# Kernel optimization log

Measured on AMD Instinct MI355X. Metric: run time of the kernel, lower is better.

The kernel has to match this reference:

```python
import jax, jax.numpy as jnp
import numpy as np

B, R, CIN, J, O, ITERS = 512, 1152, 8, 10, 16, 3  # batch, routes, in_ch, capsules, out_ch, routing iters


def squash(s, axis):
    # v = (||s||^2 / (1 + ||s||^2)) * s / ||s||  (standard CapsNet squash)
    sq = jnp.sum(s * s, axis=axis, keepdims=True)
    return (sq / (1.0 + sq)) * s * jax.lax.rsqrt(sq + 1e-8)


def setup_inputs() -> dict:
    key = jax.random.key(0)
    k1, k2 = jax.random.split(key)
    x = jax.random.normal(k1, (B, R, CIN), dtype=jnp.float32)
    W = jax.random.normal(k2, (R, J, O, CIN), dtype=jnp.float32)  # param, batch-broadcast
    return {"x": x, "W": W}


def reference(x, W):
    # u_hat[b,r,j,:] = W[r,j] @ x[b,r]   (replaces torch stack/cat broadcasting)
    u_hat = jnp.einsum('rjoc,brc->brjo', W, x)  # [B,R,J,O]
    b_ij = jnp.zeros((x.shape[0], R, J), dtype=x.dtype)
    v = None
    for it in range(ITERS):
        c_ij = jax.nn.softmax(b_ij, axis=2)                 # softmax over capsules j
        s_j = jnp.einsum('brj,brjo->bjo', c_ij, u_hat)      # weighted sum over routes
        v = squash(s_j, axis=-1)                            # [B,J,O]
        if it < ITERS - 1:
            b_ij = b_ij + jnp.einsum('brjo,bjo->brj', u_hat, v)  # agreement
    # torch returns v_j.squeeze(1) with shape [B, J, O, 1]
    return v[..., None]
```

## Files before the change

kernel.cpp:

```cpp
#include <hip/hip_runtime.h>
#include <cstdint>
#include <cstddef>

#define NB 512
#define NR 1152
#define NC 8
#define NJ 10
#define NO 16
#define NJO 160

typedef unsigned int uint32;

__device__ __forceinline__ uint32 f2bf(float f) {
    uint32 x = __float_as_uint(f);
    return (x + 0x7fffu + ((x >> 16) & 1u)) >> 16;
}
__device__ __forceinline__ float bflo(uint32 w) { return __uint_as_float(w << 16); }
__device__ __forceinline__ float bfhi(uint32 w) { return __uint_as_float(w & 0xffff0000u); }

__global__ __launch_bounds__(256) void xpose_kernel(const float* __restrict__ x,
                                                    float* __restrict__ xT) {
    const int r0 = blockIdx.x * 16;
    const int b0 = blockIdx.y * 64;
    const int t  = threadIdx.x;
    __shared__ float tile[16][65][8];

    for (int i = t; i < 2048; i += 256) {
        int b = i >> 5, r = (i >> 1) & 15, h = i & 1;
        float4 v = *(const float4*)&x[(size_t)(b0 + b) * (NR * NC) + (size_t)(r0 + r) * NC + h * 4];
        *(float4*)&tile[r][b][h * 4] = v;
    }
    __syncthreads();
    for (int i = t; i < 2048; i += 256) {
        int r = i >> 7, b = (i >> 1) & 63, h = i & 1;
        float4 v = *(const float4*)&tile[r][b][h * 4];
        *(float4*)&xT[(size_t)(r0 + r) * (NB * NC) + (size_t)(b0 + b) * NC + h * 4] = v;
    }
}

__global__ __launch_bounds__(320) void uhat_kernel(const float* __restrict__ xT,
                                                   const float* __restrict__ W,
                                                   uint32* __restrict__ u) {
    const int r = blockIdx.x;
    const int t = threadIdx.x;

    __shared__ float Ws[NC][NJO];
    __shared__ float xs[NB][NC];

    for (int i = t; i < NJO * NC; i += 320) {
        Ws[i & 7][i >> 3] = W[(size_t)r * (NJO * NC) + i];
    }
    {
        const float4* xsrc = (const float4*)(xT + (size_t)r * (NB * NC));
        float4* xdst = (float4*)&xs[0][0];
        for (int i = t; i < (NB * NC) / 4; i += 320) xdst[i] = xsrc[i];
    }
    __syncthreads();

    const int jo2  = t % 80;
    const int half = t / 80;

    float w0[8], w1[8];
#pragma unroll
    for (int c = 0; c < 8; ++c) {
        w0[c] = Ws[c][2 * jo2];
        w1[c] = Ws[c][2 * jo2 + 1];
    }

    for (int b = half; b < NB; b += 4) {
        const float4* xp = (const float4*)xs[b];
        float4 xa = xp[0], xb = xp[1];
        float a0 = w0[0] * xa.x + w0[1] * xa.y + w0[2] * xa.z + w0[3] * xa.w
                 + w0[4] * xb.x + w0[5] * xb.y + w0[6] * xb.z + w0[7] * xb.w;
        float a1 = w1[0] * xa.x + w1[1] * xa.y + w1[2] * xa.z + w1[3] * xa.w
                 + w1[4] * xb.x + w1[5] * xb.y + w1[6] * xb.z + w1[7] * xb.w;
        uint32 p = f2bf(a0) | (f2bf(a1) << 16);
        u[(size_t)(b * NR + r) * 80 + jo2] = p;
    }
}

template <int MODE>
__global__ __launch_bounds__(576, 2) void pass_kernel(const uint32* __restrict__ u,
                                                      float* __restrict__ vacc,
                                                      float* __restrict__ outp) {
    const int b  = blockIdx.x;
    const int t  = threadIdx.x;
    const int w  = t >> 6;
    const int l  = t & 63;
    const int m  = (l >> 2) & 15;
    const int qt = l & 3;

    __shared__ float vls[NJO];
    __shared__ float sl[NJO];
    for (int i = t; i < NJO; i += 576) {
        sl[i] = 0.0f;
        if (MODE != 0) vls[i] = vacc[b * NJO + i];
    }
    __syncthreads();

    float acc[40];
#pragma unroll
    for (int i = 0; i < 40; ++i) acc[i] = 0.0f;

    const uint32* ubase = u + (size_t)b * (NR * 80);

#pragma unroll 1
    for (int c8 = 0; c8 < 8; ++c8) {
        const int r = (w * 8 + c8) * 16 + m;
        const uint32* up = ubase + r * 80 + 2 * qt;

        uint32 ur[20];
#pragma unroll
        for (int j = 0; j < NJ; ++j) {
            uint2 q = *(const uint2*)(up + 8 * j);
            ur[2 * j]     = q.x;
            ur[2 * j + 1] = q.y;
        }

        float cj[NJ];
        if (MODE == 0) {
#pragma unroll
            for (int j = 0; j < NJ; ++j) cj[j] = 0.1f;
        } else {
            float sum = 0.0f;
#pragma unroll
            for (int j = 0; j < NJ; ++j) {
                float4 vv = *(const float4*)&vls[16 * j + 4 * qt];
                float pj = bflo(ur[2 * j]) * vv.x + bfhi(ur[2 * j]) * vv.y
                         + bflo(ur[2 * j + 1]) * vv.z + bfhi(ur[2 * j + 1]) * vv.w;
                pj += __shfl_xor(pj, 1);
                pj += __shfl_xor(pj, 2);
                float e = __expf(pj);
                cj[j] = e;
                sum += e;
            }
            float inv = 1.0f / sum;
#pragma unroll
            for (int j = 0; j < NJ; ++j) cj[j] *= inv;
        }

#pragma unroll
        for (int j = 0; j < NJ; ++j) {
            acc[4 * j + 0] += cj[j] * bflo(ur[2 * j]);
            acc[4 * j + 1] += cj[j] * bfhi(ur[2 * j]);
            acc[4 * j + 2] += cj[j] * bflo(ur[2 * j + 1]);
            acc[4 * j + 3] += cj[j] * bfhi(ur[2 * j + 1]);
        }
    }

    float a[24];
    {
        const int bit = (l >> 2) & 1;
#pragma unroll
        for (int i = 0; i < 24; ++i) {
            float lo = acc[i];
            float hi = (i + 24 < 40) ? acc[i + 24] : 0.0f;
            float send = bit ? lo : hi;
            float recv = __shfl_xor(send, 4);
            a[i] = (bit ? hi : lo) + recv;
        }
    }
#pragma unroll
    for (int st = 1; st < 4; ++st) {
        const int h = 24 >> st;
        const int bit = (l >> (2 + st)) & 1;
#pragma unroll
        for (int i = 0; i < 12; ++i) {
            if (i < h) {
                float send = bit ? a[i] : a[i + h];
                float recv = __shfl_xor(send, 4 << st);
                a[i] = (bit ? a[i + h] : a[i]) + recv;
            }
        }
    }
    const int base = 3 * (__brev((uint32)m) >> 28);
#pragma unroll
    for (int i = 0; i < 3; ++i) {
        int aidx = base + i;
        if (aidx < 40) {
            int j = aidx >> 2, e = aidx & 3;
            atomicAdd(&sl[16 * j + 4 * qt + e], a[i]);
        }
    }
    __syncthreads();

    if (t < 80) {
        float2 sv = *(const float2*)&sl[2 * t];
        float sq = sv.x * sv.x + sv.y * sv.y;
#pragma unroll
        for (int off = 1; off < 8; off <<= 1) sq += __shfl_xor(sq, off, 8);
        float scale = (sq / (1.0f + sq)) * rsqrtf(sq + 1e-8f);
        float vx = sv.x * scale, vy = sv.y * scale;
        if (MODE == 2) {
            *(float2*)&outp[b * NJO + 2 * t] = make_float2(vx, vy);
        } else if (MODE == 1) {
            float2 va = *(const float2*)&vacc[b * NJO + 2 * t];
            *(float2*)&vacc[b * NJO + 2 * t] = make_float2(va.x + vx, va.y + vy);
        } else {
            *(float2*)&vacc[b * NJO + 2 * t] = make_float2(vx, vy);
        }
    }
}

extern "C" void kernel_launch(void* const* d_in, const int* in_sizes, int n_in,
                              void* d_out, int out_size, void* d_ws, size_t ws_size,
                              hipStream_t stream) {
    (void)in_sizes; (void)n_in; (void)out_size; (void)ws_size;

    const float* x = (const float*)d_in[0];
    const float* W = (const float*)d_in[1];
    float* out = (float*)d_out;

    char* ws = (char*)d_ws;
    const size_t XBYTES = (size_t)NR * NB * NC * 4;
    const size_t UBYTES = (size_t)NB * NR * NJO * 2;
    float*  xT   = (float*)ws;
    uint32* u    = (uint32*)(ws + XBYTES);
    float*  vacc = (float*)(ws + XBYTES + UBYTES);

    xpose_kernel<<<dim3(NR / 16, NB / 64), 256, 0, stream>>>(x, xT);
    uhat_kernel<<<NR, 320, 0, stream>>>(xT, W, u);

    pass_kernel<0><<<NB, 576, 0, stream>>>(u, vacc, nullptr);
    pass_kernel<1><<<NB, 576, 0, stream>>>(u, vacc, nullptr);
    pass_kernel<2><<<NB, 576, 0, stream>>>(u, vacc, out);
}
```

Baseline: 231.0 us.

## Fuse three routing passes into one kernel with fp16 u_hat and vectorized loads

Merges the three per-iteration pass kernels into a single routing kernel that loops over iterations, keeping the accumulated v in shared memory instead of a global vacc buffer. u_hat is stored as fp16 instead of bf16, with the element order permuted so each thread's 20 words are contiguous and can be read with five 16-byte loads. The u_hat array is still re-read from global memory or L2 on every iteration. The aim is to remove two kernel launches and the global vacc round trips and to widen the loads. fp16 has a narrower range than bf16, which could overflow for large u_hat values.

```diff
diff --git a/kernel.cpp b/kernel.cpp
--- a/kernel.cpp
+++ b/kernel.cpp
@@ -1,4 +1,5 @@
 #include <hip/hip_runtime.h>
+#include <hip/hip_fp16.h>
 #include <cstdint>
 #include <cstddef>
 
@@ -11,12 +12,17 @@
 
 typedef unsigned int uint32;
 
-__device__ __forceinline__ uint32 f2bf(float f) {
-    uint32 x = __float_as_uint(f);
-    return (x + 0x7fffu + ((x >> 16) & 1u)) >> 16;
-}
-__device__ __forceinline__ float bflo(uint32 w) { return __uint_as_float(w << 16); }
-__device__ __forceinline__ float bfhi(uint32 w) { return __uint_as_float(w & 0xffff0000u); }
+union H2U { __half2 h; uint32 u; };
+
+__device__ __forceinline__ uint32 packf16(float a0, float a1) {
+    H2U p;
+    p.h = __halves2half2(__float2half_rn(a0), __float2half_rn(a1));
+    return p.u;
+}
+__device__ __forceinline__ float2 unpackf16(uint32 w) {
+    H2U p; p.u = w;
+    return __half22float2(p.h);
+}
 
 __global__ __launch_bounds__(256) void xpose_kernel(const float* __restrict__ x,
                                                     float* __restrict__ xT) {
@@ -44,7 +50,7 @@
     const int r = blockIdx.x;
     const int t = threadIdx.x;
 
-    __shared__ float Ws[NC][NJO];
+    __shared__ float Ws[NC][NJO + 4];
     __shared__ float xs[NB][NC];
 
     for (int i = t; i < NJO * NC; i += 320) {
@@ -57,14 +63,19 @@
     }
     __syncthreads();
 
-    const int jo2  = t % 80;
+    const int ni   = t % 80;
     const int half = t / 80;
+    const int qt  = ni / 20;
+    const int rem = ni % 20;
+    const int j   = rem >> 1;
+    const int d   = rem & 1;
+    const int jo0 = 16 * j + 4 * qt + 2 * d;
 
     float w0[8], w1[8];
 #pragma unroll
     for (int c = 0; c < 8; ++c) {
-        w0[c] = Ws[c][2 * jo2];
-        w1[c] = Ws[c][2 * jo2 + 1];
+        w0[c] = Ws[c][jo0];
+        w1[c] = Ws[c][jo0 + 1];
     }
 
     for (int b = half; b < NB; b += 4) {
@@ -74,15 +85,12 @@
                  + w0[4] * xb.x + w0[5] * xb.y + w0[6] * xb.z + w0[7] * xb.w;
         float a1 = w1[0] * xa.x + w1[1] * xa.y + w1[2] * xa.z + w1[3] * xa.w
                  + w1[4] * xb.x + w1[5] * xb.y + w1[6] * xb.z + w1[7] * xb.w;
-        uint32 p = f2bf(a0) | (f2bf(a1) << 16);
-        u[(size_t)(b * NR + r) * 80 + jo2] = p;
-    }
-}
-
-template <int MODE>
-__global__ __launch_bounds__(576, 2) void pass_kernel(const uint32* __restrict__ u,
-                                                      float* __restrict__ vacc,
-                                                      float* __restrict__ outp) {
+        u[(size_t)(b * NR + r) * 80 + ni] = packf16(a0, a1);
+    }
+}
+
+__global__ __launch_bounds__(576, 2) void routing_kernel(const uint32* __restrict__ u,
+                                                         float* __restrict__ outp) {
     const int b  = blockIdx.x;
     const int t  = threadIdx.x;
     const int w  = t >> 6;
@@ -90,114 +98,127 @@
     const int m  = (l >> 2) & 15;
     const int qt = l & 3;
 
+    __shared__ float sl[NJO];
     __shared__ float vls[NJO];
-    __shared__ float sl[NJO];
-    for (int i = t; i < NJO; i += 576) {
-        sl[i] = 0.0f;
-        if (MODE != 0) vls[i] = vacc[b * NJO + i];
-    }
+    __shared__ float vaccl[NJO];
+
+    for (int i = t; i < NJO; i += 576) sl[i] = 0.0f;
     __syncthreads();
 
-    float acc[40];
-#pragma unroll
-    for (int i = 0; i < 40; ++i) acc[i] = 0.0f;
-
-    const uint32* ubase = u + (size_t)b * (NR * 80);
+    const uint32* ubase = u + (size_t)b * (NR * 80) + qt * 20;
 
 #pragma unroll 1
-    for (int c8 = 0; c8 < 8; ++c8) {
-        const int r = (w * 8 + c8) * 16 + m;
-        const uint32* up = ubase + r * 80 + 2 * qt;
-
-        uint32 ur[20];
-#pragma unroll
-        for (int j = 0; j < NJ; ++j) {
-            uint2 q = *(const uint2*)(up + 8 * j);
-            ur[2 * j]     = q.x;
-            ur[2 * j + 1] = q.y;
-        }
-
-        float cj[NJ];
-        if (MODE == 0) {
-#pragma unroll
-            for (int j = 0; j < NJ; ++j) cj[j] = 0.1f;
-        } else {
-            float sum = 0.0f;
+    for (int it = 0; it < 3; ++it) {
+        float acc[40];
+#pragma unroll
+        for (int i = 0; i < 40; ++i) acc[i] = 0.0f;
+
+#pragma unroll 1
+        for (int c8 = 0; c8 < 8; ++c8) {
+            const int r = (w * 8 + c8) * 16 + m;
+            const uint4* up = (const uint4*)(ubase + (size_t)r * 80);
+            uint32 ur[20];
+#pragma unroll
+            for (int i = 0; i < 5; ++i) {
+                uint4 q = up[i];
+                ur[4 * i + 0] = q.x; ur[4 * i + 1] = q.y;
+                ur[4 * i + 2] = q.z; ur[4 * i + 3] = q.w;
+            }
+
+            float cj[NJ];
+            if (it == 0) {
+#pragma unroll
+                for (int j = 0; j < NJ; ++j) cj[j] = 0.1f;
+            } else {
+                float sum = 0.0f;
+#pragma unroll
+                for (int j = 0; j < NJ; ++j) {
+                    float2 ua = unpackf16(ur[2 * j]);
+                    float2 ub = unpackf16(ur[2 * j + 1]);
+                    float4 vv = *(const float4*)&vls[16 * j + 4 * qt];
+                    float pj = ua.x * vv.x + ua.y * vv.y + ub.x * vv.z + ub.y * vv.w;
+                    pj += __shfl_xor(pj, 1);
+                    pj += __shfl_xor(pj, 2);
+                    float e = __expf(pj);
+                    cj[j] = e;
+                    sum += e;
+                }
+                float inv = 1.0f / sum;
+#pragma unroll
+                for (int j = 0; j < NJ; ++j) cj[j] *= inv;
+            }
+
 #pragma unroll
             for (int j = 0; j < NJ; ++j) {
-                float4 vv = *(const float4*)&vls[16 * j + 4 * qt];
-                float pj = bflo(ur[2 * j]) * vv.x + bfhi(ur[2 * j]) * vv.y
-                         + bflo(ur[2 * j + 1]) * vv.z + bfhi(ur[2 * j + 1]) * vv.w;
-                pj += __shfl_xor(pj, 1);
-                pj += __shfl_xor(pj, 2);
-                float e = __expf(pj);
-                cj[j] = e;
-                sum += e;
-            }
-            float inv = 1.0f / sum;
-#pragma unroll
-            for (int j = 0; j < NJ; ++j) cj[j] *= inv;
-        }
-
-#pragma unroll
-        for (int j = 0; j < NJ; ++j) {
-            acc[4 * j + 0] += cj[j] * bflo(ur[2 * j]);
-            acc[4 * j + 1] += cj[j] * bfhi(ur[2 * j]);
-            acc[4 * j + 2] += cj[j] * bflo(ur[2 * j + 1]);
-            acc[4 * j + 3] += cj[j] * bfhi(ur[2 * j + 1]);
-        }
-    }
-
-    float a[24];
-    {
-        const int bit = (l >> 2) & 1;
-#pragma unroll
-        for (int i = 0; i < 24; ++i) {
-            float lo = acc[i];
-            float hi = (i + 24 < 40) ? acc[i + 24] : 0.0f;
-            float send = bit ? lo : hi;
-            float recv = __shfl_xor(send, 4);
-            a[i] = (bit ? hi : lo) + recv;
-        }
-    }
-#pragma unroll
-    for (int st = 1; st < 4; ++st) {
-        const int h = 24 >> st;
-        const int bit = (l >> (2 + st)) & 1;
-#pragma unroll
-        for (int i = 0; i < 12; ++i) {
-            if (i < h) {
-                float send = bit ? a[i] : a[i + h];
-                float recv = __shfl_xor(send, 4 << st);
-                a[i] = (bit ? a[i + h] : a[i]) + recv;
-            }
-        }
-    }
-    const int base = 3 * (__brev((uint32)m) >> 28);
-#pragma unroll
-    for (int i = 0; i < 3; ++i) {
-        int aidx = base + i;
-        if (aidx < 40) {
-            int j = aidx >> 2, e = aidx & 3;
-            atomicAdd(&sl[16 * j + 4 * qt + e], a[i]);
-        }
-    }
-    __syncthreads();
-
-    if (t < 80) {
-        float2 sv = *(const float2*)&sl[2 * t];
-        float sq = sv.x * sv.x + sv.y * sv.y;
-#pragma unroll
-        for (int off = 1; off < 8; off <<= 1) sq += __shfl_xor(sq, off, 8);
-        float scale = (sq / (1.0f + sq)) * rsqrtf(sq + 1e-8f);
-        float vx = sv.x * scale, vy = sv.y * scale;
-        if (MODE == 2) {
-            *(float2*)&outp[b * NJO + 2 * t] = make_float2(vx, vy);
-        } else if (MODE == 1) {
-            float2 va = *(const float2*)&vacc[b * NJO + 2 * t];
-            *(float2*)&vacc[b * NJO + 2 * t] = make_float2(va.x + vx, va.y + vy);
-        } else {
-            *(float2*)&vacc[b * NJO + 2 * t] = make_float2(vx, vy);
+                float2 ua = unpackf16(ur[2 * j]);
+                float2 ub = unpackf16(ur[2 * j + 1]);
+                acc[4 * j + 0] += cj[j] * ua.x;
+                acc[4 * j + 1] += cj[j] * ua.y;
+                acc[4 * j + 2] += cj[j] * ub.x;
+                acc[4 * j + 3] += cj[j] * ub.y;
+            }
+        }
+
+        float a[24];
+        {
+            const int bit = (l >> 2) & 1;
+#pragma unroll
+            for (int i = 0; i < 24; ++i) {
+                float lo = acc[i];
+                float hi = (i + 24 < 40) ? acc[i + 24] : 0.0f;
+                float send = bit ? lo : hi;
+                float recv = __shfl_xor(send, 4);
+                a[i] = (bit ? hi : lo) + recv;
+            }
+        }
+#pragma unroll
+        for (int st = 1; st < 4; ++st) {
+            const int h = 24 >> st;
+            const int bit = (l >> (2 + st)) & 1;
+#pragma unroll
+            for (int i = 0; i < 12; ++i) {
+                if (i < h) {
+                    float send = bit ? a[i] : a[i + h];
+                    float recv = __shfl_xor(send, 4 << st);
+                    a[i] = (bit ? a[i + h] : a[i]) + recv;
+                }
+            }
+        }
+        const int base = 3 * (__brev((uint32)m) >> 28);
+#pragma unroll
+        for (int i = 0; i < 3; ++i) {
+            int aidx = base + i;
+            if (aidx < 40) {
+                int j = aidx >> 2, e = aidx & 3;
+                atomicAdd(&sl[16 * j + 4 * qt + e], a[i]);
+            }
+        }
+        __syncthreads();
+
+        if (t < 80) {
+            float2 sv = *(const float2*)&sl[2 * t];
+            float sq = sv.x * sv.x + sv.y * sv.y;
+#pragma unroll
+            for (int off = 1; off < 8; off <<= 1) sq += __shfl_xor(sq, off, 8);
+            float scale = (sq / (1.0f + sq)) * rsqrtf(sq + 1e-8f);
+            float vx = sv.x * scale, vy = sv.y * scale;
+            if (it == 2) {
+                *(float2*)&outp[b * NJO + 2 * t] = make_float2(vx, vy);
+            } else {
+                float2 va;
+                if (it == 0) va = make_float2(vx, vy);
+                else {
+                    va = *(const float2*)&vaccl[2 * t];
+                    va.x += vx; va.y += vy;
+                }
+                *(float2*)&vaccl[2 * t] = va;
+                *(float2*)&vls[2 * t]   = va;
+            }
+        }
+        __syncthreads();
+        if (it < 2) {
+            for (int i = t; i < NJO; i += 576) sl[i] = 0.0f;
+            __syncthreads();
         }
     }
 }
@@ -213,15 +234,10 @@
 
     char* ws = (char*)d_ws;
     const size_t XBYTES = (size_t)NR * NB * NC * 4;
-    const size_t UBYTES = (size_t)NB * NR * NJO * 2;
-    float*  xT   = (float*)ws;
-    uint32* u    = (uint32*)(ws + XBYTES);
-    float*  vacc = (float*)(ws + XBYTES + UBYTES);
+    float*  xT = (float*)ws;
+    uint32* u  = (uint32*)(ws + XBYTES);
 
     xpose_kernel<<<dim3(NR / 16, NB / 64), 256, 0, stream>>>(x, xT);
     uhat_kernel<<<NR, 320, 0, stream>>>(xT, W, u);
-
-    pass_kernel<0><<<NB, 576, 0, stream>>>(u, vacc, nullptr);
-    pass_kernel<1><<<NB, 576, 0, stream>>>(u, vacc, nullptr);
-    pass_kernel<2><<<NB, 576, 0, stream>>>(u, vacc, out);
-}
+    routing_kernel<<<NB, 576, 0, stream>>>(u, out);
+}
```

Result: faster. 219.4 us (-5.0%).
